# Optimization experiments

Measured on AMD Instinct MI355X. Metric: run time of the kernel, lower is better.

Reference implementation:

```python
import jax, jax.numpy as jnp
import numpy as np

N_FEATURE = 40
EMBED_DIM = 64
HIDDEN = 64
OUT_DIM = 1
BATCH = 2048

# pairwise indices (i<j), fixed constants
_ROW, _COL = np.triu_indices(N_FEATURE, k=1)
ROW = jnp.asarray(_ROW)
COL = jnp.asarray(_COL)


def setup_inputs() -> dict:
    key = jax.random.key(0)
    ks = jax.random.split(key, 7)
    s_e = 1.0 / np.sqrt(EMBED_DIM)
    s_h = 1.0 / np.sqrt(HIDDEN)
    return {
        "x": jax.random.normal(ks[0], (BATCH, N_FEATURE, EMBED_DIM), jnp.float32),
        "W1": jax.random.uniform(ks[1], (HIDDEN, EMBED_DIM), jnp.float32, -s_e, s_e),
        "b1": jax.random.uniform(ks[2], (HIDDEN,), jnp.float32, -s_e, s_e),
        "W2": jax.random.uniform(ks[3], (1, HIDDEN), jnp.float32, -s_h, s_h),
        "b2": jax.random.uniform(ks[4], (1,), jnp.float32, -s_h, s_h),
        "Wl": jax.random.uniform(ks[5], (OUT_DIM, EMBED_DIM), jnp.float32, -s_e, s_e),
        "bl": jax.random.uniform(ks[6], (OUT_DIM,), jnp.float32, -s_e, s_e),
    }


def reference(x, W1, b1, W2, b2, Wl, bl):
    # pairwise elementwise products: [B, P, E]
    p = x[:, ROW, :]
    q = x[:, COL, :]
    inner = p * q
    # small attention MLP: Linear -> ReLU -> Linear -> softmax over pairs dim
    h = jax.nn.relu(jnp.einsum('bpe,he->bph', inner, W1) + b1)
    logits = jnp.einsum('bph,oh->bpo', h, W2) + b2  # [B, P, 1]
    attn = jax.nn.softmax(logits, axis=1)
    # softmax-weighted sum over pairs -> [B, E]
    pooled = jnp.sum(inner * attn, axis=1)
    # final linear (dropout p=0 is identity)
    return pooled @ Wl.T + bl
```

## Files before the change

### kernel.cpp

```cpp
#include <hip/hip_runtime.h>
#include <math.h>

#define NF 40
#define ED 64
#define NP 780
#define GPB 4
#define BT 512
#define NTT 49

typedef __attribute__((ext_vector_type(8))) _Float16 f16x8;
typedef __attribute__((ext_vector_type(2))) __fp16  fp16x2;
typedef __attribute__((ext_vector_type(4))) float   f32x4;

__global__ __launch_bounds__(BT, 2)
void afm_mfma16j_kernel(const float* __restrict__ x,
                        const float* __restrict__ W1,
                        const float* __restrict__ b1,
                        const float* __restrict__ W2,
                        const float* __restrict__ Wl,
                        const float* __restrict__ blp,
                        float* __restrict__ out)
{
    __shared__ __align__(16) unsigned char sxh[GPB * NF * 128];
    __shared__ __align__(16) unsigned char sfrag[10 * 64 * 16];
    __shared__ unsigned int srctw[800];
    __shared__ float sred[8][2];

    const int tid  = threadIdx.x;
    const int lane = tid & 63;
    const int w    = tid >> 6;
    const int gb   = w >> 1;
    const int half = w & 1;
    const int ln15 = lane & 15;
    const int g    = lane >> 4;
    const int cg   = g << 4;

    const int b0 = blockIdx.x * GPB + gb;
    unsigned char* sxw = sxh + gb * (NF * 128);

    {
        const float4* xg = (const float4*)(x + (size_t)b0 * NF * ED);
        const int llp = half * 64 + lane;
        #pragma unroll
        for (int i = 0; i < 5; ++i) {
            const int u = llp + i * 128;
            float4 v = xg[u];
            const int r = u >> 4, j = u & 15;
            union { fp16x2 h2[2]; unsigned long long ll; } pk;
            pk.h2[0] = __builtin_amdgcn_cvt_pkrtz(v.x, v.y);
            pk.h2[1] = __builtin_amdgcn_cvt_pkrtz(v.z, v.w);
            const int byteoff = r * 128 + (((j >> 1) ^ (r & 7)) << 4) + (j & 1) * 8;
            *(unsigned long long*)(sxw + byteoff) = pk.ll;
        }
    }

    for (int slot = tid; slot < 640; slot += BT) {
        const int f = slot >> 6, l = slot & 63;
        const int lg = l >> 4, l15 = l & 15;
        const float* src = (f < 8)
            ? (W1 + ((f >> 1) * 16 + l15) * ED + (f & 1) * 32 + lg * 8)
            : (Wl + (f - 8) * 32 + lg * 8);
        union { fp16x2 h2[4]; f16x8 h8; } u;
        u.h2[0] = __builtin_amdgcn_cvt_pkrtz(src[0], src[1]);
        u.h2[1] = __builtin_amdgcn_cvt_pkrtz(src[2], src[3]);
        u.h2[2] = __builtin_amdgcn_cvt_pkrtz(src[4], src[5]);
        u.h2[3] = __builtin_amdgcn_cvt_pkrtz(src[6], src[7]);
        *(f16x8*)(sfrag + slot * 16) = u.h8;
    }
    for (int p = tid; p < 800; p += BT) {
        const int pq = p < NP ? p : NP - 1;
        const int r = (int)((79.0f - sqrtf(6241.0f - 8.0f * (float)pq)) * 0.5f);
        const int c = pq - ((r * (79 - r)) >> 1) + r + 1;
        const unsigned int er = (unsigned int)((r << 7) | ((r & 7) << 4));
        const unsigned int ec = (unsigned int)((c << 7) | ((c & 7) << 4));
        srctw[p] = er | (ec << 16);
    }

    f32x4  b1v[4];
    fp16x2 w2h[4][2];
    #pragma unroll
    for (int mf = 0; mf < 4; ++mf) {
        float4 wv = *(const float4*)(W2 + mf * 16 + g * 4);
        b1v[mf] = *(const f32x4*)(b1 + mf * 16 + g * 4);
        const float L2E = 1.4426950408889634f;
        w2h[mf][0] = __builtin_amdgcn_cvt_pkrtz(wv.x * L2E, wv.y * L2E);
        w2h[mf][1] = __builtin_amdgcn_cvt_pkrtz(wv.z * L2E, wv.w * L2E);
    }
    const float blv = blp[0];

    __syncthreads();

    f16x8 Ah[4][2], Awl[2];
    #pragma unroll
    for (int mf = 0; mf < 4; ++mf)
        #pragma unroll
        for (int ks = 0; ks < 2; ++ks)
            Ah[mf][ks] = *(const f16x8*)(sfrag + ((mf * 2 + ks) * 64 + lane) * 16);
    #pragma unroll
    for (int ks = 0; ks < 2; ++ks)
        Awl[ks] = *(const f16x8*)(sfrag + ((8 + ks) * 64 + lane) * 16);

    const f32x4 zero4 = {0.f, 0.f, 0.f, 0.f};
    const fp16x2 zh = {(__fp16)0.f, (__fp16)0.f};

    const int t0 = half ? 25 : 0;
    const int t1 = half ? NTT : 25;

    unsigned int rc = srctw[t0 * 16 + ln15];
    int offr = (int)(rc & 0xffffu) ^ cg;
    int offc = (int)(rc >> 16) ^ cg;
    f16x8 xr0 = *(const f16x8*)(sxw + offr);
    f16x8 xr1 = *(const f16x8*)(sxw + (offr ^ 64));
    f16x8 xc0 = *(const f16x8*)(sxw + offc);
    f16x8 xc1 = *(const f16x8*)(sxw + (offc ^ 64));

    float le = 0.f, les = 0.f;
    for (int tile = t0; tile < t1; ++tile) {
        const unsigned int rcn = srctw[(tile + 1) * 16 + ln15];
        const int offrn = (int)(rcn & 0xffffu) ^ cg;
        const int offcn = (int)(rcn >> 16) ^ cg;
        f16x8 nr0 = *(const f16x8*)(sxw + offrn);
        f16x8 nr1 = *(const f16x8*)(sxw + (offrn ^ 64));
        f16x8 nc0 = *(const f16x8*)(sxw + offcn);
        f16x8 nc1 = *(const f16x8*)(sxw + (offcn ^ 64));

        f16x8 Bf0 = xr0 * xc0;
        f16x8 Bf1 = xr1 * xc1;

        f32x4 sacc;
        sacc = __builtin_amdgcn_mfma_f32_16x16x32_f16(Awl[0], Bf0, zero4, 0, 0, 0);
        sacc = __builtin_amdgcn_mfma_f32_16x16x32_f16(Awl[1], Bf1, sacc, 0, 0, 0);

        f32x4 acc[4];
        #pragma unroll
        for (int mf = 0; mf < 4; ++mf) {
            acc[mf] = __builtin_amdgcn_mfma_f32_16x16x32_f16(Ah[mf][0], Bf0, b1v[mf], 0, 0, 0);
            acc[mf] = __builtin_amdgcn_mfma_f32_16x16x32_f16(Ah[mf][1], Bf1, acc[mf], 0, 0, 0);
        }

        float q0 = 0.f, q1 = 0.f;
        #pragma unroll
        for (int mf = 0; mf < 4; ++mf) {
            fp16x2 h01 = __builtin_amdgcn_cvt_pkrtz(acc[mf][0], acc[mf][1]);
            fp16x2 h23 = __builtin_amdgcn_cvt_pkrtz(acc[mf][2], acc[mf][3]);
            h01 = __builtin_elementwise_max(h01, zh);
            h23 = __builtin_elementwise_max(h23, zh);
            if (mf & 1) {
                q1 = __builtin_amdgcn_fdot2(h01, w2h[mf][0], q1, false);
                q1 = __builtin_amdgcn_fdot2(h23, w2h[mf][1], q1, false);
            } else {
                q0 = __builtin_amdgcn_fdot2(h01, w2h[mf][0], q0, false);
                q0 = __builtin_amdgcn_fdot2(h23, w2h[mf][1], q0, false);
            }
        }
        float part = q0 + q1;
        part += __shfl_xor(part, 16);
        part += __shfl_xor(part, 32);

        const int p = tile * 16 + ln15;
        const float e_ = (p < NP) ? exp2f(part) : 0.f;
        le  += e_;
        les  = fmaf(e_, sacc[0], les);

        xr0 = nr0; xr1 = nr1; xc0 = nc0; xc1 = nc1;
    }

    #pragma unroll
    for (int off = 1; off < 16; off <<= 1) {
        le  += __shfl_xor(le, off);
        les += __shfl_xor(les, off);
    }
    if (lane == 0) { sred[w][0] = le; sred[w][1] = les; }
    __syncthreads();

    if (half == 0 && lane == 0) {
        const float E  = sred[w][0] + sred[w + 1][0];
        const float ES = sred[w][1] + sred[w + 1][1];
        out[b0] = ES / E + blv;
    }
}

extern "C" void kernel_launch(void* const* d_in, const int* in_sizes, int n_in,
                              void* d_out, int out_size, void* d_ws, size_t ws_size,
                              hipStream_t stream) {
    const float* x  = (const float*)d_in[0];
    const float* W1 = (const float*)d_in[1];
    const float* b1 = (const float*)d_in[2];
    const float* W2 = (const float*)d_in[3];
    const float* Wl = (const float*)d_in[5];
    const float* bl = (const float*)d_in[6];
    float* out = (float*)d_out;

    const int B = in_sizes[0] / (NF * ED);
    afm_mfma16j_kernel<<<B / GPB, BT, 0, stream>>>(x, W1, b1, W2, Wl, bl, out);
}
```

Measured before the change: 26.46 us.

## Split each batch row's pair tiles across four waves instead of two

Halves the batch rows per block so each row's 49 pair tiles are split over four waves (13/12/12/12) instead of two. The grid doubles to 1024 blocks, giving more parallelism on a 256-CU device and shorter per-wave loops. The software prefetch of the next tile's LDS operands is dropped in favour of direct loads each iteration, and the weight-fragment conversion overhead is now paid per 2 rows instead of 4.

```diff
diff --git a/kernel.cpp b/kernel.cpp
--- a/kernel.cpp
+++ b/kernel.cpp
@@ -4,7 +4,7 @@
 #define NF 40
 #define ED 64
 #define NP 780
-#define GPB 4
+#define GPB 2
 #define BT 512
 #define NTT 49
 
@@ -13,7 +13,7 @@
 typedef __attribute__((ext_vector_type(4))) float   f32x4;
 
 __global__ __launch_bounds__(BT, 2)
-void afm_mfma16j_kernel(const float* __restrict__ x,
+void afm_mfma16l_kernel(const float* __restrict__ x,
                         const float* __restrict__ W1,
                         const float* __restrict__ b1,
                         const float* __restrict__ W2,
@@ -23,14 +23,14 @@
 {
     __shared__ __align__(16) unsigned char sxh[GPB * NF * 128];
     __shared__ __align__(16) unsigned char sfrag[10 * 64 * 16];
-    __shared__ unsigned int srctw[800];
+    __shared__ unsigned int srctw[784];
     __shared__ float sred[8][2];
 
     const int tid  = threadIdx.x;
     const int lane = tid & 63;
     const int w    = tid >> 6;
-    const int gb   = w >> 1;
-    const int half = w & 1;
+    const int gb   = w >> 2;
+    const int q    = w & 3;
     const int ln15 = lane & 15;
     const int g    = lane >> 4;
     const int cg   = g << 4;
@@ -40,17 +40,19 @@
 
     {
         const float4* xg = (const float4*)(x + (size_t)b0 * NF * ED);
-        const int llp = half * 64 + lane;
+        const int base = q * 64 + lane;
         #pragma unroll
-        for (int i = 0; i < 5; ++i) {
-            const int u = llp + i * 128;
-            float4 v = xg[u];
-            const int r = u >> 4, j = u & 15;
-            union { fp16x2 h2[2]; unsigned long long ll; } pk;
-            pk.h2[0] = __builtin_amdgcn_cvt_pkrtz(v.x, v.y);
-            pk.h2[1] = __builtin_amdgcn_cvt_pkrtz(v.z, v.w);
-            const int byteoff = r * 128 + (((j >> 1) ^ (r & 7)) << 4) + (j & 1) * 8;
-            *(unsigned long long*)(sxw + byteoff) = pk.ll;
+        for (int i = 0; i < 3; ++i) {
+            const int u = base + i * 256;
+            if (u < NF * 16) {
+                float4 v = xg[u];
+                const int r = u >> 4, j = u & 15;
+                union { fp16x2 h2[2]; unsigned long long ll; } pk;
+                pk.h2[0] = __builtin_amdgcn_cvt_pkrtz(v.x, v.y);
+                pk.h2[1] = __builtin_amdgcn_cvt_pkrtz(v.z, v.w);
+                const int byteoff = r * 128 + (((j >> 1) ^ (r & 7)) << 4) + (j & 1) * 8;
+                *(unsigned long long*)(sxw + byteoff) = pk.ll;
+            }
         }
     }
 
@@ -67,7 +69,7 @@
         u.h2[3] = __builtin_amdgcn_cvt_pkrtz(src[6], src[7]);
         *(f16x8*)(sfrag + slot * 16) = u.h8;
     }
-    for (int p = tid; p < 800; p += BT) {
+    for (int p = tid; p < 784; p += BT) {
         const int pq = p < NP ? p : NP - 1;
         const int r = (int)((79.0f - sqrtf(6241.0f - 8.0f * (float)pq)) * 0.5f);
         const int c = pq - ((r * (79 - r)) >> 1) + r + 1;
@@ -103,27 +105,19 @@
     const f32x4 zero4 = {0.f, 0.f, 0.f, 0.f};
     const fp16x2 zh = {(__fp16)0.f, (__fp16)0.f};
 
-    const int t0 = half ? 25 : 0;
-    const int t1 = half ? NTT : 25;
-
-    unsigned int rc = srctw[t0 * 16 + ln15];
-    int offr = (int)(rc & 0xffffu) ^ cg;
-    int offc = (int)(rc >> 16) ^ cg;
-    f16x8 xr0 = *(const f16x8*)(sxw + offr);
-    f16x8 xr1 = *(const f16x8*)(sxw + (offr ^ 64));
-    f16x8 xc0 = *(const f16x8*)(sxw + offc);
-    f16x8 xc1 = *(const f16x8*)(sxw + (offc ^ 64));
+    const int t0 = q == 0 ? 0 : 13 + 12 * (q - 1);
+    const int t1 = t0 + (q == 0 ? 13 : 12);
 
     float le = 0.f, les = 0.f;
     for (int tile = t0; tile < t1; ++tile) {
-        const unsigned int rcn = srctw[(tile + 1) * 16 + ln15];
-        const int offrn = (int)(rcn & 0xffffu) ^ cg;
-        const int offcn = (int)(rcn >> 16) ^ cg;
-        f16x8 nr0 = *(const f16x8*)(sxw + offrn);
-        f16x8 nr1 = *(const f16x8*)(sxw + (offrn ^ 64));
-        f16x8 nc0 = *(const f16x8*)(sxw + offcn);
-        f16x8 nc1 = *(const f16x8*)(sxw + (offcn ^ 64));
-
+        const int p = tile * 16 + ln15;
+        const unsigned int rc = srctw[p];
+        const int offr = (int)(rc & 0xffffu) ^ cg;
+        const int offc = (int)(rc >> 16) ^ cg;
+        f16x8 xr0 = *(const f16x8*)(sxw + offr);
+        f16x8 xr1 = *(const f16x8*)(sxw + (offr ^ 64));
+        f16x8 xc0 = *(const f16x8*)(sxw + offc);
+        f16x8 xc1 = *(const f16x8*)(sxw + (offc ^ 64));
         f16x8 Bf0 = xr0 * xc0;
         f16x8 Bf1 = xr1 * xc1;
 
@@ -157,12 +151,9 @@
         part += __shfl_xor(part, 16);
         part += __shfl_xor(part, 32);
 
-        const int p = tile * 16 + ln15;
         const float e_ = (p < NP) ? exp2f(part) : 0.f;
         le  += e_;
         les  = fmaf(e_, sacc[0], les);
-
-        xr0 = nr0; xr1 = nr1; xc0 = nc0; xc1 = nc1;
     }
 
     #pragma unroll
@@ -173,9 +164,9 @@
     if (lane == 0) { sred[w][0] = le; sred[w][1] = les; }
     __syncthreads();
 
-    if (half == 0 && lane == 0) {
-        const float E  = sred[w][0] + sred[w + 1][0];
-        const float ES = sred[w][1] + sred[w + 1][1];
+    if (q == 0 && lane == 0) {
+        const float E  = sred[w][0] + sred[w + 1][0] + sred[w + 2][0] + sred[w + 3][0];
+        const float ES = sred[w][1] + sred[w + 1][1] + sred[w + 2][1] + sred[w + 3][1];
         out[b0] = ES / E + blv;
     }
 }
@@ -192,5 +183,5 @@
     float* out = (float*)d_out;
 
     const int B = in_sizes[0] / (NF * ED);
-    afm_mfma16j_kernel<<<B / GPB, BT, 0, stream>>>(x, W1, b1, W2, Wl, bl, out);
+    afm_mfma16l_kernel<<<B / GPB, BT, 0, stream>>>(x, W1, b1, W2, Wl, bl, out);
 }
```

Measured after the change: 27.35 us. 1.03x slower.
